# Optimization experiments

Hardware: AMD Instinct MI355X
Metric: run time of the kernel (lower is better)

The kernel has to match this reference:

```python
import jax, jax.numpy as jnp
import numpy as np


def setup_inputs() -> dict:
    key = jax.random.key(0)
    k1, k2 = jax.random.split(key)
    N, P1, P2, D = 4, 8192, 8192, 3
    source_cloud = jax.random.normal(k1, (N, P1, D), dtype=jnp.float32)
    target_cloud = jax.random.normal(k2, (N, P2, D), dtype=jnp.float32)
    return {"source_cloud": source_cloud, "target_cloud": target_cloud}


def reference(source_cloud, target_cloud):
    # ChamferDistance.forward with defaults:
    #   bidirectional=False, reverse=False -> single-directional x->y
    #   point_reduction='sum', batch_reduction='mean', norm=2, no normals/weights
    x, y = source_cloud, target_cloud  # (N,P1,D), (N,P2,D)
    x2 = jnp.sum(x * x, axis=-1)                       # (N,P1)
    y2 = jnp.sum(y * y, axis=-1)                       # (N,P2)
    xy = jnp.einsum('npd,nqd->npq', x, y)              # (N,P1,P2)
    d2 = x2[:, :, None] + y2[None if False else slice(None), None, :] - 2.0 * xy  # (N,P1,P2)
    # squared L2 distances are non-negative; clamp tiny negatives from the GEMM trick
    nn_d2 = jnp.maximum(jnp.min(d2, axis=-1), 0.0)     # (N,P1) 1-NN squared dist
    per_cloud = jnp.sum(nn_d2, axis=1)                 # point_reduction='sum'
    loss = jnp.mean(per_cloud)                         # batch_reduction='mean'
    return loss
```

## Files before the change

kernel.cpp:

```cpp
#include <hip/hip_runtime.h>
#include <float.h>

#define N_BATCH 4
#define P1 8192
#define P2 8192
#define D 3

#define CHUNK 256
#define NCHUNK (P2 / CHUNK)
#define RSRC 8
#define TPB 256
#define SRC_PER_BLK (TPB * RSRC)
#define NSRCBLK (P1 / SRC_PER_BLK)
#define NMIN (N_BATCH * P1)

__global__ void chamfer_init_mins(unsigned* __restrict__ mins) {
    int i = blockIdx.x * blockDim.x + threadIdx.x;
    if (i < NMIN) mins[i] = 0x7F7FFFFFu;
}

__global__ __launch_bounds__(TPB) void chamfer_main(
        const float* __restrict__ src,
        const float* __restrict__ tgt,
        unsigned* __restrict__ mins) {
    const int bid = blockIdx.x;
    const int c   = bid % NCHUNK;
    const int sb  = (bid / NCHUNK) % NSRCBLK;
    const int n   = bid / (NCHUNK * NSRCBLK);
    const int t   = threadIdx.x;

    __shared__ float4 sT[CHUNK];

    {
        const int j = c * CHUNK + t;
        const float* p = tgt + ((size_t)n * P2 + j) * D;
        const float y0 = p[0], y1 = p[1], y2 = p[2];
        sT[t] = make_float4(-2.0f * y0, -2.0f * y1, -2.0f * y2,
                            y0 * y0 + y1 * y1 + y2 * y2);
    }
    __syncthreads();

    float x0[RSRC], x1[RSRC], x2[RSRC], xsq[RSRC], m[RSRC];
#pragma unroll
    for (int i = 0; i < RSRC; ++i) {
        const int s = sb * SRC_PER_BLK + i * TPB + t;
        const float* p = src + ((size_t)n * P1 + s) * D;
        x0[i] = p[0]; x1[i] = p[1]; x2[i] = p[2];
        xsq[i] = x0[i] * x0[i] + x1[i] * x1[i] + x2[i] * x2[i];
        m[i] = FLT_MAX;
    }

#pragma unroll 4
    for (int j = 0; j < CHUNK; ++j) {
        const float4 y = sT[j];
#pragma unroll
        for (int i = 0; i < RSRC; ++i) {
            float d = __builtin_fmaf(x0[i], y.x, y.w);
            d = __builtin_fmaf(x1[i], y.y, d);
            d = __builtin_fmaf(x2[i], y.z, d);
            m[i] = fminf(m[i], d);
        }
    }

#pragma unroll
    for (int i = 0; i < RSRC; ++i) {
        const int s = sb * SRC_PER_BLK + i * TPB + t;
        const float v = fmaxf(xsq[i] + m[i], 0.0f);
        atomicMin(&mins[n * P1 + s], __float_as_uint(v));
    }
}

__global__ void chamfer_reduce(const float* __restrict__ mins,
                               float* __restrict__ out) {
    const int tid = blockIdx.x * blockDim.x + threadIdx.x;
    float v = 0.0f;
    for (int i = tid; i < NMIN; i += gridDim.x * blockDim.x)
        v += mins[i];
#pragma unroll
    for (int off = 32; off > 0; off >>= 1)
        v += __shfl_down(v, off, 64);
    __shared__ float sred[TPB / 64];
    const int lane = threadIdx.x & 63;
    const int w    = threadIdx.x >> 6;
    if (lane == 0) sred[w] = v;
    __syncthreads();
    if (threadIdx.x == 0) {
        float s = 0.0f;
#pragma unroll
        for (int i = 0; i < TPB / 64; ++i) s += sred[i];
        atomicAdd(out, s * (1.0f / N_BATCH));
    }
}

extern "C" void kernel_launch(void* const* d_in, const int* in_sizes, int n_in,
                              void* d_out, int out_size, void* d_ws, size_t ws_size,
                              hipStream_t stream) {
    const float* src = (const float*)d_in[0];
    const float* tgt = (const float*)d_in[1];
    float* out = (float*)d_out;
    unsigned* mins = (unsigned*)d_ws;

    hipMemsetAsync(out, 0, sizeof(float), stream);

    chamfer_init_mins<<<(NMIN + TPB - 1) / TPB, TPB, 0, stream>>>(mins);

    const int nblocks = N_BATCH * NSRCBLK * NCHUNK;
    chamfer_main<<<nblocks, TPB, 0, stream>>>(src, tgt, mins);

    chamfer_reduce<<<64, TPB, 0, stream>>>((const float*)mins, out);
}
```

Measured before the change: 35.89 us.

## Replace atomicMin scatter with per-chunk partial min buffer and fused reduce

Each main-kernel block now writes its per-chunk partial minima to a workspace slice indexed by chunk, instead of doing atomicMin into a shared array. The reduce kernel takes the min over all 32 chunks per point, adds the source squared norm, clamps, and sums. This removes the init kernel and the atomic contention. It costs 32x more workspace traffic (about 4 MB written and read) and needs a larger workspace. The inner loop is also restructured to process two targets per iteration with a combined min.

```diff
diff --git a/kernel.cpp b/kernel.cpp
--- a/kernel.cpp
+++ b/kernel.cpp
@@ -14,15 +14,10 @@
 #define NSRCBLK (P1 / SRC_PER_BLK)
 #define NMIN (N_BATCH * P1)
 
-__global__ void chamfer_init_mins(unsigned* __restrict__ mins) {
-    int i = blockIdx.x * blockDim.x + threadIdx.x;
-    if (i < NMIN) mins[i] = 0x7F7FFFFFu;
-}
-
 __global__ __launch_bounds__(TPB) void chamfer_main(
         const float* __restrict__ src,
         const float* __restrict__ tgt,
-        unsigned* __restrict__ mins) {
+        float* __restrict__ ws) {
     const int bid = blockIdx.x;
     const int c   = bid % NCHUNK;
     const int sb  = (bid / NCHUNK) % NSRCBLK;
@@ -40,42 +35,53 @@
     }
     __syncthreads();
 
-    float x0[RSRC], x1[RSRC], x2[RSRC], xsq[RSRC], m[RSRC];
+    float x0[RSRC], x1[RSRC], x2[RSRC], m[RSRC];
 #pragma unroll
     for (int i = 0; i < RSRC; ++i) {
         const int s = sb * SRC_PER_BLK + i * TPB + t;
         const float* p = src + ((size_t)n * P1 + s) * D;
         x0[i] = p[0]; x1[i] = p[1]; x2[i] = p[2];
-        xsq[i] = x0[i] * x0[i] + x1[i] * x1[i] + x2[i] * x2[i];
         m[i] = FLT_MAX;
     }
 
-#pragma unroll 4
-    for (int j = 0; j < CHUNK; ++j) {
-        const float4 y = sT[j];
+#pragma unroll 2
+    for (int j = 0; j < CHUNK; j += 2) {
+        const float4 ya = sT[j];
+        const float4 yb = sT[j + 1];
 #pragma unroll
         for (int i = 0; i < RSRC; ++i) {
-            float d = __builtin_fmaf(x0[i], y.x, y.w);
-            d = __builtin_fmaf(x1[i], y.y, d);
-            d = __builtin_fmaf(x2[i], y.z, d);
-            m[i] = fminf(m[i], d);
+            float da = __builtin_fmaf(x0[i], ya.x, ya.w);
+            da = __builtin_fmaf(x1[i], ya.y, da);
+            da = __builtin_fmaf(x2[i], ya.z, da);
+            float db = __builtin_fmaf(x0[i], yb.x, yb.w);
+            db = __builtin_fmaf(x1[i], yb.y, db);
+            db = __builtin_fmaf(x2[i], yb.z, db);
+            m[i] = fminf(fminf(m[i], da), db);
         }
     }
 
 #pragma unroll
     for (int i = 0; i < RSRC; ++i) {
-        const int s = sb * SRC_PER_BLK + i * TPB + t;
-        const float v = fmaxf(xsq[i] + m[i], 0.0f);
-        atomicMin(&mins[n * P1 + s], __float_as_uint(v));
+        const int s = n * P1 + sb * SRC_PER_BLK + i * TPB + t;
+        ws[(size_t)c * NMIN + s] = m[i];
     }
 }
 
-__global__ void chamfer_reduce(const float* __restrict__ mins,
-                               float* __restrict__ out) {
-    const int tid = blockIdx.x * blockDim.x + threadIdx.x;
-    float v = 0.0f;
-    for (int i = tid; i < NMIN; i += gridDim.x * blockDim.x)
-        v += mins[i];
+__global__ __launch_bounds__(TPB) void chamfer_reduce(
+        const float* __restrict__ ws,
+        const float* __restrict__ src,
+        float* __restrict__ out) {
+    const int gid = blockIdx.x * TPB + threadIdx.x;
+
+    float v = ws[gid];
+#pragma unroll
+    for (int c = 1; c < NCHUNK; ++c)
+        v = fminf(v, ws[(size_t)c * NMIN + gid]);
+
+    const float* p = src + (size_t)gid * D;
+    const float xs = p[0] * p[0] + p[1] * p[1] + p[2] * p[2];
+    v = fmaxf(v + xs, 0.0f);
+
 #pragma unroll
     for (int off = 32; off > 0; off >>= 1)
         v += __shfl_down(v, off, 64);
@@ -98,14 +104,12 @@
     const float* src = (const float*)d_in[0];
     const float* tgt = (const float*)d_in[1];
     float* out = (float*)d_out;
-    unsigned* mins = (unsigned*)d_ws;
+    float* ws  = (float*)d_ws;
 
     hipMemsetAsync(out, 0, sizeof(float), stream);
 
-    chamfer_init_mins<<<(NMIN + TPB - 1) / TPB, TPB, 0, stream>>>(mins);
+    const int nblocks = N_BATCH * NSRCBLK * NCHUNK;
+    chamfer_main<<<nblocks, TPB, 0, stream>>>(src, tgt, ws);
 
-    const int nblocks = N_BATCH * NSRCBLK * NCHUNK;
-    chamfer_main<<<nblocks, TPB, 0, stream>>>(src, tgt, mins);
-
-    chamfer_reduce<<<64, TPB, 0, stream>>>((const float*)mins, out);
+    chamfer_reduce<<<NMIN / TPB, TPB, 0, stream>>>(ws, src, out);
 }
```

Result: slower. 37.80 us (+5.3%).

## Replace brute-force NN search with x-binned spatial pruning

Applied to the files above, without the earlier changes.

Targets are scattered into 64 x-axis bins with a fixed per-bin capacity. Each wave then searches one source point's bin and expands outward, stopping once the 1D distance bound exceeds the current best. This removes most of the all-pairs distance work and the atomicMin pass, and a direct store plus a vectorized reduce replace them. The per-bin capacity assumes roughly Gaussian-distributed inputs and could overflow on other data, and the pruning adds divergent, serialized per-wave work.

```diff
diff --git a/kernel.cpp b/kernel.cpp
--- a/kernel.cpp
+++ b/kernel.cpp
@@ -4,90 +4,108 @@
 #define N_BATCH 4
 #define P1 8192
 #define P2 8192
-#define D 3
 
-#define CHUNK 256
-#define NCHUNK (P2 / CHUNK)
-#define RSRC 8
-#define TPB 256
-#define SRC_PER_BLK (TPB * RSRC)
-#define NSRCBLK (P1 / SRC_PER_BLK)
+#define NB 64
+#define BW 0.125f
+#define BINV 8.0f
+#define CAP 1024
 #define NMIN (N_BATCH * P1)
+#define NWAVES 8192
 
-__global__ void chamfer_init_mins(unsigned* __restrict__ mins) {
-    int i = blockIdx.x * blockDim.x + threadIdx.x;
-    if (i < NMIN) mins[i] = 0x7F7FFFFFu;
+
+__global__ __launch_bounds__(256) void chamfer_scatter(
+        const float* __restrict__ tgt,
+        int* __restrict__ cursor,
+        float4* __restrict__ pk,
+        float* __restrict__ out) {
+    const int i = blockIdx.x * 256 + threadIdx.x;
+    if (i == 0) out[0] = 0.0f;
+    const int n = i >> 13;
+    const float* p = tgt + (size_t)i * 3;
+    const float x = p[0], y = p[1], z = p[2];
+    int b = (int)((x + 4.0f) * BINV);
+    b = min(max(b, 0), NB - 1);
+    const int g = (n << 6) + b;
+    const int r = atomicAdd(&cursor[g], 1);
+    pk[((size_t)g << 10) + r] =
+        make_float4(-2.0f * x, -2.0f * y, -2.0f * z, x * x + y * y + z * z);
 }
 
-__global__ __launch_bounds__(TPB) void chamfer_main(
+__global__ __launch_bounds__(256) void chamfer_main(
         const float* __restrict__ src,
-        const float* __restrict__ tgt,
-        unsigned* __restrict__ mins) {
-    const int bid = blockIdx.x;
-    const int c   = bid % NCHUNK;
-    const int sb  = (bid / NCHUNK) % NSRCBLK;
-    const int n   = bid / (NCHUNK * NSRCBLK);
-    const int t   = threadIdx.x;
-
-    __shared__ float4 sT[CHUNK];
-
-    {
-        const int j = c * CHUNK + t;
-        const float* p = tgt + ((size_t)n * P2 + j) * D;
-        const float y0 = p[0], y1 = p[1], y2 = p[2];
-        sT[t] = make_float4(-2.0f * y0, -2.0f * y1, -2.0f * y2,
-                            y0 * y0 + y1 * y1 + y2 * y2);
-    }
-    __syncthreads();
-
-    float x0[RSRC], x1[RSRC], x2[RSRC], xsq[RSRC], m[RSRC];
-#pragma unroll
-    for (int i = 0; i < RSRC; ++i) {
-        const int s = sb * SRC_PER_BLK + i * TPB + t;
-        const float* p = src + ((size_t)n * P1 + s) * D;
-        x0[i] = p[0]; x1[i] = p[1]; x2[i] = p[2];
-        xsq[i] = x0[i] * x0[i] + x1[i] * x1[i] + x2[i] * x2[i];
-        m[i] = FLT_MAX;
-    }
-
-#pragma unroll 4
-    for (int j = 0; j < CHUNK; ++j) {
-        const float4 y = sT[j];
-#pragma unroll
-        for (int i = 0; i < RSRC; ++i) {
-            float d = __builtin_fmaf(x0[i], y.x, y.w);
-            d = __builtin_fmaf(x1[i], y.y, d);
-            d = __builtin_fmaf(x2[i], y.z, d);
-            m[i] = fminf(m[i], d);
-        }
-    }
+        const int* __restrict__ cursor,
+        const float4* __restrict__ pk,
+        float* __restrict__ mins) {
+    const int lane = threadIdx.x & 63;
+    const int gw = blockIdx.x * 4 + (threadIdx.x >> 6);
 
 #pragma unroll
-    for (int i = 0; i < RSRC; ++i) {
-        const int s = sb * SRC_PER_BLK + i * TPB + t;
-        const float v = fmaxf(xsq[i] + m[i], 0.0f);
-        atomicMin(&mins[n * P1 + s], __float_as_uint(v));
+    for (int n = 0; n < N_BATCH; ++n) {
+        const int s = gw + (n << 13);
+        const float* ps = src + (size_t)s * 3;
+        const float xs = ps[0], ys = ps[1], zs = ps[2];
+        const float xsq = xs * xs + ys * ys + zs * zs;
+        const int b = min(max((int)((xs + 4.0f) * BINV), 0), NB - 1);
+        float m = FLT_MAX;
+
+        {
+            const int g = (n << 6) + b;
+            const int cnt = cursor[g];
+            const float4* base = pk + ((size_t)g << 10);
+            for (int j = lane; j < cnt; j += 64) {
+                const float4 q = base[j];
+                float d = fmaf(xs, q.x, q.w);
+                d = fmaf(ys, q.y, d);
+                d = fmaf(zs, q.z, d);
+                m = fminf(m, d);
+            }
+        }
+
+        int bR = b + 1, bL = b - 1;
+        while (true) {
+            const float lbR = (bR < NB) ? (bR * BW - 4.0f - xs) : 1e30f;
+            const float lbL = (bL >= 0) ? (xs - ((bL + 1) * BW - 4.0f)) : 1e30f;
+            float lb = fminf(lbR, lbL);
+            if (lb > 1e29f) break;
+            lb *= 0.999f;
+            if (__any(m + xsq <= lb * lb)) break;
+            const int bb = (lbR <= lbL) ? bR : bL;
+            if (lbR <= lbL) ++bR; else --bL;
+            const int g = (n << 6) + bb;
+            const int cnt = cursor[g];
+            const float4* base = pk + ((size_t)g << 10);
+            for (int j = lane; j < cnt; j += 64) {
+                const float4 q = base[j];
+                float d = fmaf(xs, q.x, q.w);
+                d = fmaf(ys, q.y, d);
+                d = fmaf(zs, q.z, d);
+                m = fminf(m, d);
+            }
+        }
+
+#pragma unroll
+        for (int off = 32; off > 0; off >>= 1)
+            m = fminf(m, __shfl_xor(m, off, 64));
+        if (lane == 0) mins[s] = fmaxf(m + xsq, 0.0f);
     }
 }
 
-__global__ void chamfer_reduce(const float* __restrict__ mins,
-                               float* __restrict__ out) {
-    const int tid = blockIdx.x * blockDim.x + threadIdx.x;
-    float v = 0.0f;
-    for (int i = tid; i < NMIN; i += gridDim.x * blockDim.x)
-        v += mins[i];
+__global__ __launch_bounds__(256) void chamfer_reduce(
+        const float4* __restrict__ mins4,
+        float* __restrict__ out) {
+    const int i = blockIdx.x * 256 + threadIdx.x;
+    const float4 v = mins4[i];
+    float r = (v.x + v.y) + (v.z + v.w);
 #pragma unroll
     for (int off = 32; off > 0; off >>= 1)
-        v += __shfl_down(v, off, 64);
-    __shared__ float sred[TPB / 64];
+        r += __shfl_down(r, off, 64);
+    __shared__ float sred[4];
     const int lane = threadIdx.x & 63;
     const int w    = threadIdx.x >> 6;
-    if (lane == 0) sred[w] = v;
+    if (lane == 0) sred[w] = r;
     __syncthreads();
     if (threadIdx.x == 0) {
-        float s = 0.0f;
-#pragma unroll
-        for (int i = 0; i < TPB / 64; ++i) s += sred[i];
+        float s = (sred[0] + sred[1]) + (sred[2] + sred[3]);
         atomicAdd(out, s * (1.0f / N_BATCH));
     }
 }
@@ -98,14 +116,16 @@
     const float* src = (const float*)d_in[0];
     const float* tgt = (const float*)d_in[1];
     float* out = (float*)d_out;
-    unsigned* mins = (unsigned*)d_ws;
 
-    hipMemsetAsync(out, 0, sizeof(float), stream);
+    int*    cursor = (int*)d_ws;
+    float4* pk     = (float4*)((char*)d_ws + 4096);
+    float*  mins   = (float*)((char*)d_ws + 4096 + (size_t)N_BATCH * NB * CAP * 16);
 
-    chamfer_init_mins<<<(NMIN + TPB - 1) / TPB, TPB, 0, stream>>>(mins);
+    hipMemsetAsync(cursor, 0, N_BATCH * NB * sizeof(int), stream);
 
-    const int nblocks = N_BATCH * NSRCBLK * NCHUNK;
-    chamfer_main<<<nblocks, TPB, 0, stream>>>(src, tgt, mins);
+    chamfer_scatter<<<NMIN / 256, 256, 0, stream>>>(tgt, cursor, pk, out);
 
-    chamfer_reduce<<<64, TPB, 0, stream>>>((const float*)mins, out);
+    chamfer_main<<<NWAVES / 4, 256, 0, stream>>>(src, cursor, pk, mins);
+
+    chamfer_reduce<<<NMIN / 4 / 256, 256, 0, stream>>>((const float4*)mins, out);
 }
```

New measurement: 64.87 us. 1.81x slower.
